# Kernel tuning notes

Hardware: AMD Instinct MI355X
Metric: run time of the kernel (lower is better)

Reference implementation:

```python
import jax, jax.numpy as jnp
import numpy as np
import math

H = 32      # num attention heads
KV = 8      # num key/value heads
D = 64      # head dim
ROPE_BASE = 10000.0


def _rope_cos_sin(seq_len, dtype):
    inv_freq = 1.0 / (ROPE_BASE ** (jnp.arange(0, D, 2, dtype=jnp.float32) / D))
    t = jnp.arange(seq_len, dtype=jnp.float32)
    freqs = jnp.einsum('i,j->ij', t, inv_freq)          # [S, D/2]
    emb = jnp.concatenate([freqs, freqs], axis=-1)       # [S, D]
    return jnp.cos(emb).astype(dtype)[None, None], jnp.sin(emb).astype(dtype)[None, None]


def _rotate_half(x):
    x1, x2 = x[..., : D // 2], x[..., D // 2:]
    return jnp.concatenate([-x2, x1], axis=-1)


def setup_inputs() -> dict:
    key = jax.random.key(0)
    ks = jax.random.split(key, 5)
    B, S, Hid = 1, 2048, 2048
    hidden_states = jax.random.normal(ks[0], (B, S, Hid), dtype=jnp.float32)
    Wq = jax.random.normal(ks[1], (Hid, H * D), dtype=jnp.float32) * (1.0 / math.sqrt(Hid))
    Wk = jax.random.normal(ks[2], (Hid, KV * D), dtype=jnp.float32) * (1.0 / math.sqrt(Hid))
    Wv = jax.random.normal(ks[3], (Hid, KV * D), dtype=jnp.float32) * (1.0 / math.sqrt(Hid))
    Wo = jax.random.normal(ks[4], (H * D, Hid), dtype=jnp.float32) * (1.0 / math.sqrt(H * D))
    # additive causal mask
    causal = jnp.tril(jnp.ones((S, S), dtype=bool))
    attention_mask = jnp.where(causal, 0.0, -1e9).astype(jnp.float32)[None, None]
    return {"hidden_states": hidden_states, "Wq": Wq, "Wk": Wk, "Wv": Wv,
            "Wo": Wo, "attention_mask": attention_mask}


def reference(hidden_states, Wq, Wk, Wv, Wo, attention_mask):
    B, S, _ = hidden_states.shape
    groups = H // KV
    # projections -> [B, heads, S, D]
    q = (hidden_states @ Wq).reshape(B, S, H, D).transpose(0, 2, 1, 3)
    k = (hidden_states @ Wk).reshape(B, S, KV, D).transpose(0, 2, 1, 3)
    v = (hidden_states @ Wv).reshape(B, S, KV, D).transpose(0, 2, 1, 3)
    # RoPE
    cos, sin = _rope_cos_sin(S, q.dtype)
    q = q * cos + _rotate_half(q) * sin
    k = k * cos + _rotate_half(k) * sin
    # GQA head expansion (repeat_interleave along head axis)
    k = jnp.repeat(k, groups, axis=1)
    v = jnp.repeat(v, groups, axis=1)
    # scaled dot-product attention (eager)
    scores = jnp.einsum('bhqd,bhkd->bhqk', q, k) / math.sqrt(D)
    scores = scores + attention_mask
    probs = jax.nn.softmax(scores.astype(jnp.float32), axis=-1).astype(q.dtype)
    attn = jnp.einsum('bhqk,bhkd->bhqd', probs, v)
    attn = attn.transpose(0, 2, 1, 3).reshape(B, S, H * D)
    return attn @ Wo
```

## Files before the change

kernel.cpp:

```cpp
#include <hip/hip_runtime.h>
#include <hip/hip_bf16.h>
#include <math.h>

#define S_LEN 2048
#define HID   2048
#define NH    32
#define NKV   8
#define HD    64
#define KVW   (NKV * HD)

typedef __attribute__((ext_vector_type(8))) short bf16x8;
typedef __attribute__((ext_vector_type(4))) float f32x4;
typedef unsigned short u16;

__device__ __forceinline__ u16 f2bf(float f) {
    return (u16)((__builtin_bit_cast(unsigned, f) + 0x8000u) >> 16);
}
__device__ __forceinline__ float bf2f(u16 v) {
    unsigned u = ((unsigned)v) << 16;
    return __builtin_bit_cast(float, u);
}
__device__ __forceinline__ unsigned pack2bf(float a, float b) {
    unsigned ua = __builtin_bit_cast(unsigned, a) + 0x8000u;
    unsigned ub = __builtin_bit_cast(unsigned, b) + 0x8000u;
    return (ua >> 16) | (ub & 0xFFFF0000u);
}
__device__ __forceinline__ void stage16(const u16* g, u16* lds_base) {
    __builtin_amdgcn_global_load_lds((const __attribute__((address_space(1))) void*)g,
                                     (__attribute__((address_space(3))) void*)lds_base, 16, 0, 0);
}

__global__ __launch_bounds__(256) void cvt_bf16x8_kernel(const float* __restrict__ X,
                                                         u16* __restrict__ Y, int n8) {
    int i = blockIdx.x * 256 + threadIdx.x;
    if (i >= n8) return;
    const float4* p = (const float4*)(X + (size_t)i * 8);
    float4 a = p[0], b = p[1];
    uint4 o;
    o.x = pack2bf(a.x, a.y);
    o.y = pack2bf(a.z, a.w);
    o.z = pack2bf(b.x, b.y);
    o.w = pack2bf(b.z, b.w);
    *(uint4*)(Y + (size_t)i * 8) = o;
}

__global__ __launch_bounds__(256) void transpose_cvt4(const float* __restrict__ Wq,
                                                      const float* __restrict__ Wk,
                                                      const float* __restrict__ Wv,
                                                      const float* __restrict__ Wo,
                                                      u16* __restrict__ WqkvT,
                                                      u16* __restrict__ WoT) {
    const float* X; u16* Y; int C;
    const int z = blockIdx.z;
    if (z == 0)      { X = Wq; Y = WqkvT;                        C = HID; }
    else if (z == 1) { X = Wo; Y = WoT;                          C = HID; }
    else if (z == 2) { X = Wk; Y = WqkvT + (size_t)2048 * HID;   C = KVW; }
    else             { X = Wv; Y = WqkvT + (size_t)2560 * HID;   C = KVW; }
    const int c0 = blockIdx.x * 32, r0 = blockIdx.y * 32;
    if (c0 >= C) return;
    __shared__ float T[32][33];
    const int tx = threadIdx.x & 31, ty = threadIdx.x >> 5;
#pragma unroll
    for (int i = 0; i < 4; i++)
        T[ty + 8 * i][tx] = X[(size_t)(r0 + ty + 8 * i) * C + c0 + tx];
    __syncthreads();
#pragma unroll
    for (int i = 0; i < 4; i++)
        Y[(size_t)(c0 + ty + 8 * i) * HID + r0 + tx] = f2bf(T[tx][ty + 8 * i]);
}

template <int EPI>
__global__ __launch_bounds__(512, 2) void gemm_bf16(const u16* __restrict__ A,
                                                    const u16* __restrict__ Bt,
                                                    float* __restrict__ C,
                                                    u16* __restrict__ Qh,
                                                    u16* __restrict__ Kh,
                                                    u16* __restrict__ Vt) {
    constexpr int KTOT = 2048;
    constexpr int NT = KTOT / 32;
    constexpr int SLOT = 12288;
    __shared__ u16 smem[4 * SLOT];

    const int tiles = gridDim.x * gridDim.y;
    const int flat = blockIdx.y * gridDim.x + blockIdx.x;
    const int per = tiles >> 3;
    const int swz = (flat & 7) * per + (flat >> 3);
    const int bxx = swz % gridDim.x, byy = swz / gridDim.x;
    const int bm = byy * 128, bn = bxx * 256;

    const int tid = threadIdx.x;
    const int w = tid >> 6, lane = tid & 63;
    const int qd = lane >> 4, r = lane & 15;
    const int wm = w >> 2, wn = w & 3;

    f32x4 acc[4][4];
#pragma unroll
    for (int m = 0; m < 4; m++)
#pragma unroll
        for (int n = 0; n < 4; n++) {
            acc[m][n][0] = 0.f; acc[m][n][1] = 0.f;
            acc[m][n][2] = 0.f; acc[m][n][3] = 0.f;
        }

    auto stage_tile = [&](int kt) {
        u16* slot = smem + (size_t)(kt & 3) * SLOT;
        const int k0 = kt * 32;
        const u16* ga = A + (size_t)(bm + w * 16 + r) * KTOT + k0 + qd * 8;
        stage16(ga, slot + w * 512);
        const u16* gb0 = Bt + (size_t)(bn + w * 16 + r) * KTOT + k0 + qd * 8;
        stage16(gb0, slot + 4096 + w * 512);
        const u16* gb1 = Bt + (size_t)(bn + (w + 8) * 16 + r) * KTOT + k0 + qd * 8;
        stage16(gb1, slot + 4096 + (w + 8) * 512);
    };

    auto compute_tile = [&](int kt) {
        const u16* slot = smem + (size_t)(kt & 3) * SLOT;
        bf16x8 af[4], bfv[4];
#pragma unroll
        for (int m = 0; m < 4; m++)
            af[m] = *(const bf16x8*)&slot[(wm * 4 + m) * 512 + lane * 8];
#pragma unroll
        for (int n = 0; n < 4; n++)
            bfv[n] = *(const bf16x8*)&slot[4096 + (wn * 4 + n) * 512 + lane * 8];
        __builtin_amdgcn_s_setprio(1);
#pragma unroll
        for (int m = 0; m < 4; m++)
#pragma unroll
            for (int n = 0; n < 4; n++)
                acc[m][n] = __builtin_amdgcn_mfma_f32_16x16x32_bf16(af[m], bfv[n], acc[m][n], 0, 0, 0);
        __builtin_amdgcn_s_setprio(0);
    };

#define VMB(n_) do { asm volatile("s_waitcnt vmcnt(" #n_ ")" ::: "memory");  \
                     __builtin_amdgcn_s_barrier();                           \
                     __builtin_amdgcn_sched_barrier(0); } while (0)

    stage_tile(0);
    stage_tile(1);
    stage_tile(2);

    for (int kt = 0; kt < NT - 3; ++kt) {
        VMB(6);
        stage_tile(kt + 3);
        __builtin_amdgcn_sched_barrier(0);
        compute_tile(kt);
    }
    VMB(6); compute_tile(NT - 3);
    VMB(3); compute_tile(NT - 2);
    VMB(0); compute_tile(NT - 1);
#undef VMB

    const int row0 = bm + wm * 64;
    const int col0 = bn + wn * 64;
    if (EPI == 0) {
#pragma unroll
        for (int m = 0; m < 4; m++)
#pragma unroll
            for (int n = 0; n < 4; n++)
#pragma unroll
                for (int reg = 0; reg < 4; reg++)
                    C[(size_t)(row0 + m * 16 + qd * 4 + reg) * HID + col0 + n * 16 + r] =
                        acc[m][n][reg];
    } else if (bn < 2048) {
#pragma unroll
        for (int m = 0; m < 4; m++)
#pragma unroll
            for (int n = 0; n < 4; n++)
#pragma unroll
                for (int reg = 0; reg < 4; reg++)
                    Qh[(size_t)(row0 + m * 16 + qd * 4 + reg) * HID + col0 + n * 16 + r] =
                        f2bf(acc[m][n][reg]);
    } else if (bn < 2560) {
        const int hb = (bn - 2048) + wn * 64;
#pragma unroll
        for (int n = 0; n < 2; n++) {
            const int c0 = n * 16 + r;
            const float inv = __expf(-(float)c0 * 0.2878231366242596f);
#pragma unroll
            for (int m = 0; m < 4; m++)
#pragma unroll
                for (int reg = 0; reg < 4; reg++) {
                    int srow = row0 + m * 16 + qd * 4 + reg;
                    float ang = (float)srow * inv;
                    float cs = cosf(ang), sn = sinf(ang);
                    float k1 = acc[m][n][reg], k2 = acc[m][n + 2][reg];
                    size_t o = (size_t)srow * KVW + hb + c0;
                    Kh[o]      = f2bf(k1 * cs - k2 * sn);
                    Kh[o + 32] = f2bf(k2 * cs + k1 * sn);
                }
        }
    } else {
#pragma unroll
        for (int m = 0; m < 4; m++)
#pragma unroll
            for (int n = 0; n < 4; n++) {
                int nrel = (bn - 2560) + wn * 64 + n * 16 + r;
                int m0 = row0 + m * 16 + qd * 4;
                ushort4 v;
                v.x = f2bf(acc[m][n][0]); v.y = f2bf(acc[m][n][1]);
                v.z = f2bf(acc[m][n][2]); v.w = f2bf(acc[m][n][3]);
                *(ushort4*)(Vt + (size_t)nrel * S_LEN + m0) = v;
            }
    }
}

__global__ __launch_bounds__(512, 6) void attn_mfma(const u16* __restrict__ Qh,
                                                    const u16* __restrict__ K,
                                                    const u16* __restrict__ Vt,
                                                    u16* __restrict__ O) {
    __shared__ u16 Kbuf[2][4096];
    __shared__ u16 Vbuf[4096];
    __shared__ u16 P_lds[8][16][72];

    const int w    = threadIdx.x >> 6;
    const int lane = threadIdx.x & 63;
    const int qd   = lane >> 4;
    const int r    = lane & 15;
    const int qb   = 15 - (int)blockIdx.x;
    const int h    = blockIdx.y;
    const int kvh  = h >> 2;
    const int q0w  = qb * 128 + w * 16;

    const u16* qrow = Qh + (size_t)(q0w + r) * (NH * HD) + h * HD;
    bf16x8 qlo = *(const bf16x8*)(qrow + qd * 8);
    bf16x8 qhi = *(const bf16x8*)(qrow + 32 + qd * 8);
    float y1[8], y2[8];
    const float spos = (float)(q0w + r);
    const float LN1E4_OVER_32 = 0.2878231366242596f;
#pragma unroll
    for (int i = 0; i < 8; i++) {
        int jj = qd * 8 + i;
        float x1 = bf2f((u16)qlo[i]);
        float x2 = bf2f((u16)qhi[i]);
        float inv = __expf(-(float)jj * LN1E4_OVER_32);
        float ang = spos * inv;
        float c = cosf(ang), sn = sinf(ang);
        y1[i] = (x1 * c - x2 * sn) * 0.125f;
        y2[i] = (x2 * c + x1 * sn) * 0.125f;
    }
    bf16x8 qfrag[2];
    {
        union { unsigned u[4]; bf16x8 v; } a, b;
#pragma unroll
        for (int i = 0; i < 4; i++) {
            a.u[i] = pack2bf(y1[2 * i], y1[2 * i + 1]);
            b.u[i] = pack2bf(y2[2 * i], y2[2 * i + 1]);
        }
        qfrag[0] = a.v; qfrag[1] = b.v;
    }

    bf16x8 ones;
    {
        union { u16 s[8]; bf16x8 v; } u;
#pragma unroll
        for (int i = 0; i < 8; i++) u.s[i] = 0x3F80;
        ones = u.v;
    }

    f32x4 oacc[4];
    f32x4 lacc;
#pragma unroll
    for (int i = 0; i < 4; i++) { oacc[i][0]=0.f; oacc[i][1]=0.f; oacc[i][2]=0.f; oacc[i][3]=0.f; }
    lacc[0]=0.f; lacc[1]=0.f; lacc[2]=0.f; lacc[3]=0.f;

    const int ktmax = 2 * qb + 1;

#define STAGE_K(kt_, buf_)                                                        \
    {                                                                             \
        const u16* g = K + (size_t)((kt_) * 64 + (w >> 1) * 16 + r) * KVW         \
                         + kvh * HD + (w & 1) * 32 + qd * 8;                      \
        stage16(g, &Kbuf[buf_][w * 512]);                                         \
    }
#define STAGE_V(kt_)                                                              \
    {                                                                             \
        const u16* g = Vt + (size_t)(kvh * HD + (w >> 1) * 16 + r) * S_LEN        \
                          + (kt_) * 64 + (w & 1) * 32 + qd * 8;                   \
        stage16(g, &Vbuf[w * 512]);                                               \
    }

    STAGE_K(0, 0);
    __syncthreads();
    int cur = 0;

    for (int kt = 0; kt <= ktmax; kt++) {
        STAGE_V(kt);
        if (kt < ktmax) STAGE_K(kt + 1, cur ^ 1);

        f32x4 s[4];
#pragma unroll
        for (int nt = 0; nt < 4; nt++) {
            bf16x8 kf0 = *(const bf16x8*)&Kbuf[cur][(nt * 2 + 0) * 512 + lane * 8];
            bf16x8 kf1 = *(const bf16x8*)&Kbuf[cur][(nt * 2 + 1) * 512 + lane * 8];
            f32x4 z; z[0]=0.f; z[1]=0.f; z[2]=0.f; z[3]=0.f;
            z = __builtin_amdgcn_mfma_f32_16x16x32_bf16(qfrag[0], kf0, z, 0, 0, 0);
            s[nt] = __builtin_amdgcn_mfma_f32_16x16x32_bf16(qfrag[1], kf1, z, 0, 0, 0);
        }

        if (kt * 64 + 63 > q0w) {
#pragma unroll
            for (int nt = 0; nt < 4; nt++) {
                int key = kt * 64 + nt * 16 + r;
#pragma unroll
                for (int reg = 0; reg < 4; reg++) {
                    int qg = q0w + qd * 4 + reg;
                    if (key > qg) s[nt][reg] = -1e30f;
                }
            }
        }

#pragma unroll
        for (int nt = 0; nt < 4; nt++)
#pragma unroll
            for (int reg = 0; reg < 4; reg++)
                P_lds[w][qd * 4 + reg][nt * 16 + r] = f2bf(__expf(s[nt][reg]));

        __syncthreads();

#pragma unroll
        for (int c = 0; c < 2; c++) {
            bf16x8 pf = *(const bf16x8*)&P_lds[w][r][c * 32 + qd * 8];
            lacc = __builtin_amdgcn_mfma_f32_16x16x32_bf16(pf, ones, lacc, 0, 0, 0);
#pragma unroll
            for (int ntd = 0; ntd < 4; ntd++) {
                bf16x8 vf = *(const bf16x8*)&Vbuf[(ntd * 2 + c) * 512 + lane * 8];
                oacc[ntd] = __builtin_amdgcn_mfma_f32_16x16x32_bf16(pf, vf, oacc[ntd], 0, 0, 0);
            }
        }

        __syncthreads();
        cur ^= 1;
    }
#undef STAGE_K
#undef STAGE_V

    float rl[4];
#pragma unroll
    for (int reg = 0; reg < 4; reg++) rl[reg] = 1.f / lacc[reg];
#pragma unroll
    for (int ntd = 0; ntd < 4; ntd++)
#pragma unroll
        for (int reg = 0; reg < 4; reg++)
            O[(size_t)(q0w + qd * 4 + reg) * (NH * HD) + h * HD + ntd * 16 + r] =
                f2bf(oacc[ntd][reg] * rl[reg]);
}

extern "C" void kernel_launch(void* const* d_in, const int* in_sizes, int n_in,
                              void* d_out, int out_size, void* d_ws, size_t ws_size,
                              hipStream_t stream) {
    const float* hidden = (const float*)d_in[0];
    const float* Wq = (const float*)d_in[1];
    const float* Wk = (const float*)d_in[2];
    const float* Wv = (const float*)d_in[3];
    const float* Wo = (const float*)d_in[4];
    float* out = (float*)d_out;

    char* ws = (char*)d_ws;
    const size_t MB = 1024 * 1024;
    u16* Hh     = (u16*)(ws + 0 * MB);
    u16* WqkvT  = (u16*)(ws + 8 * MB);
    u16* WoT    = (u16*)(ws + 20 * MB);
    u16* Qh     = (u16*)(ws + 28 * MB);
    u16* Kh     = (u16*)(ws + 36 * MB);
    u16* Vt     = (u16*)(ws + 38 * MB);
    u16* Ob     = WqkvT;

    cvt_bf16x8_kernel<<<(S_LEN * HID / 8 + 255) / 256, 256, 0, stream>>>(hidden, Hh, S_LEN * HID / 8);
    transpose_cvt4<<<dim3(HID / 32, HID / 32, 4), 256, 0, stream>>>(Wq, Wk, Wv, Wo, WqkvT, WoT);

    gemm_bf16<1><<<dim3(3072 / 256, S_LEN / 128), 512, 0, stream>>>(Hh, WqkvT, nullptr, Qh, Kh, Vt);

    attn_mfma<<<dim3(S_LEN / 128, NH), 512, 0, stream>>>(Qh, Kh, Vt, Ob);

    gemm_bf16<0><<<dim3(HID / 256, S_LEN / 128), 512, 0, stream>>>(Ob, WoT, out, nullptr, nullptr, nullptr);
}
```

Measured before the change: 288.8 us.

## Enlarge GEMM block tile to 256x256 with 64-wide K double buffering

Both GEMMs now use 256x256 output tiles per block, with 8x4 MFMA accumulators per warp, instead of 128x256. The 4-stage, 32-wide K ring buffer is replaced by a double-buffered 64-wide K stage using full vmcnt(0) waits and barriers. The aim is more operand reuse per LDS load and fewer loop iterations. In exchange the grid shrinks to 96 and 64 blocks, fewer than the CU count. LDS use also rises to 128KB, which limits occupancy and latency hiding.

```diff
diff --git a/kernel.cpp b/kernel.cpp
--- a/kernel.cpp
+++ b/kernel.cpp
@@ -75,86 +75,99 @@
                                                     float* __restrict__ C,
                                                     u16* __restrict__ Qh,
                                                     u16* __restrict__ Kh,
-                                                    u16* __restrict__ Vt) {
-    constexpr int KTOT = 2048;
-    constexpr int NT = KTOT / 32;
-    constexpr int SLOT = 12288;
-    __shared__ u16 smem[4 * SLOT];
+                                                    u16* __restrict__ Vt,
+                                                    int K) {
+    __shared__ u16 As[2][16384];
+    __shared__ u16 Bs[2][16384];
 
     const int tiles = gridDim.x * gridDim.y;
     const int flat = blockIdx.y * gridDim.x + blockIdx.x;
     const int per = tiles >> 3;
     const int swz = (flat & 7) * per + (flat >> 3);
     const int bxx = swz % gridDim.x, byy = swz / gridDim.x;
-    const int bm = byy * 128, bn = bxx * 256;
-
-    const int tid = threadIdx.x;
-    const int w = tid >> 6, lane = tid & 63;
+    const int bm = byy * 256, bn = bxx * 256;
+
+    const int t = threadIdx.x;
+    const int w = t >> 6, lane = t & 63;
     const int qd = lane >> 4, r = lane & 15;
     const int wm = w >> 2, wn = w & 3;
-
-    f32x4 acc[4][4];
-#pragma unroll
-    for (int m = 0; m < 4; m++)
+    const bool kblk = (EPI == 1) && (bn >= 2048) && (bn < 2560);
+    const int NT = K >> 6;
+
+    f32x4 acc[8][4];
+#pragma unroll
+    for (int m = 0; m < 8; m++)
 #pragma unroll
         for (int n = 0; n < 4; n++) {
             acc[m][n][0] = 0.f; acc[m][n][1] = 0.f;
             acc[m][n][2] = 0.f; acc[m][n][3] = 0.f;
         }
 
-    auto stage_tile = [&](int kt) {
-        u16* slot = smem + (size_t)(kt & 3) * SLOT;
-        const int k0 = kt * 32;
-        const u16* ga = A + (size_t)(bm + w * 16 + r) * KTOT + k0 + qd * 8;
-        stage16(ga, slot + w * 512);
-        const u16* gb0 = Bt + (size_t)(bn + w * 16 + r) * KTOT + k0 + qd * 8;
-        stage16(gb0, slot + 4096 + w * 512);
-        const u16* gb1 = Bt + (size_t)(bn + (w + 8) * 16 + r) * KTOT + k0 + qd * 8;
-        stage16(gb1, slot + 4096 + (w + 8) * 512);
-    };
-
-    auto compute_tile = [&](int kt) {
-        const u16* slot = smem + (size_t)(kt & 3) * SLOT;
-        bf16x8 af[4], bfv[4];
-#pragma unroll
-        for (int m = 0; m < 4; m++)
-            af[m] = *(const bf16x8*)&slot[(wm * 4 + m) * 512 + lane * 8];
-#pragma unroll
-        for (int n = 0; n < 4; n++)
-            bfv[n] = *(const bf16x8*)&slot[4096 + (wn * 4 + n) * 512 + lane * 8];
-        __builtin_amdgcn_s_setprio(1);
-#pragma unroll
-        for (int m = 0; m < 4; m++)
-#pragma unroll
-            for (int n = 0; n < 4; n++)
-                acc[m][n] = __builtin_amdgcn_mfma_f32_16x16x32_bf16(af[m], bfv[n], acc[m][n], 0, 0, 0);
-        __builtin_amdgcn_s_setprio(0);
-    };
-
-#define VMB(n_) do { asm volatile("s_waitcnt vmcnt(" #n_ ")" ::: "memory");  \
-                     __builtin_amdgcn_s_barrier();                           \
-                     __builtin_amdgcn_sched_barrier(0); } while (0)
-
-    stage_tile(0);
-    stage_tile(1);
-    stage_tile(2);
-
-    for (int kt = 0; kt < NT - 3; ++kt) {
-        VMB(6);
-        stage_tile(kt + 3);
-        __builtin_amdgcn_sched_barrier(0);
-        compute_tile(kt);
-    }
-    VMB(6); compute_tile(NT - 3);
-    VMB(3); compute_tile(NT - 2);
-    VMB(0); compute_tile(NT - 1);
-#undef VMB
-
-    const int row0 = bm + wm * 64;
+#define STAGE_TILE(kt_, s_)                                                       \
+    {                                                                             \
+        const int k0_ = (kt_) * 64;                                               \
+        _Pragma("unroll")                                                         \
+        for (int l = 0; l < 4; l++) {                                             \
+            const int chunk = w * 4 + l;                                          \
+            const int tt = chunk >> 1, ss = chunk & 1;                            \
+            const u16* ga = A + (size_t)(bm + tt * 16 + r) * K + k0_ + ss * 32 + qd * 8; \
+            stage16(ga, &As[s_][chunk * 512]);                                    \
+            const u16* gb = Bt + (size_t)(bn + tt * 16 + r) * K + k0_ + ss * 32 + qd * 8; \
+            stage16(gb, &Bs[s_][chunk * 512]);                                    \
+        }                                                                         \
+    }
+
+#define QUAD(s_, qm_, qn_)                                                        \
+    {                                                                             \
+        bf16x8 af[4][2], bfv[2][2];                                               \
+        _Pragma("unroll")                                                         \
+        for (int i = 0; i < 4; i++)                                               \
+            _Pragma("unroll")                                                     \
+            for (int kk = 0; kk < 2; kk++)                                        \
+                af[i][kk] = *(const bf16x8*)&As[s_][((wm * 8 + (qm_) * 4 + i) * 2 + kk) * 512 + lane * 8]; \
+        _Pragma("unroll")                                                         \
+        for (int j = 0; j < 2; j++)                                               \
+            _Pragma("unroll")                                                     \
+            for (int kk = 0; kk < 2; kk++)                                        \
+                bfv[j][kk] = *(const bf16x8*)&Bs[s_][((wn * 4 + (qn_) * 2 + j) * 2 + kk) * 512 + lane * 8]; \
+        __builtin_amdgcn_s_setprio(1);                                            \
+        _Pragma("unroll")                                                         \
+        for (int i = 0; i < 4; i++)                                               \
+            _Pragma("unroll")                                                     \
+            for (int j = 0; j < 2; j++)                                           \
+                _Pragma("unroll")                                                 \
+                for (int kk = 0; kk < 2; kk++)                                    \
+                    acc[(qm_) * 4 + i][(qn_) * 2 + j] =                           \
+                        __builtin_amdgcn_mfma_f32_16x16x32_bf16(af[i][kk], bfv[j][kk], \
+                            acc[(qm_) * 4 + i][(qn_) * 2 + j], 0, 0, 0);          \
+        __builtin_amdgcn_s_setprio(0);                                            \
+    }
+
+#define WAITBAR                                                                   \
+    asm volatile("s_waitcnt vmcnt(0)" ::: "memory");                              \
+    __builtin_amdgcn_s_barrier();
+
+    STAGE_TILE(0, 0);
+    WAITBAR;
+
+    for (int i2 = 0; i2 < NT / 2; ++i2) {
+        const int te = 2 * i2;
+        STAGE_TILE(te + 1, 1);
+        QUAD(0, 0, 0) QUAD(0, 0, 1) QUAD(0, 1, 0) QUAD(0, 1, 1)
+        WAITBAR;
+        if (te + 2 < NT) STAGE_TILE(te + 2, 0);
+        QUAD(1, 0, 0) QUAD(1, 0, 1) QUAD(1, 1, 0) QUAD(1, 1, 1)
+        WAITBAR;
+    }
+#undef STAGE_TILE
+#undef QUAD
+#undef WAITBAR
+
+    const int row0 = bm + wm * 128;
     const int col0 = bn + wn * 64;
     if (EPI == 0) {
 #pragma unroll
-        for (int m = 0; m < 4; m++)
+        for (int m = 0; m < 8; m++)
 #pragma unroll
             for (int n = 0; n < 4; n++)
 #pragma unroll
@@ -163,21 +176,21 @@
                         acc[m][n][reg];
     } else if (bn < 2048) {
 #pragma unroll
-        for (int m = 0; m < 4; m++)
+        for (int m = 0; m < 8; m++)
 #pragma unroll
             for (int n = 0; n < 4; n++)
 #pragma unroll
                 for (int reg = 0; reg < 4; reg++)
                     Qh[(size_t)(row0 + m * 16 + qd * 4 + reg) * HID + col0 + n * 16 + r] =
                         f2bf(acc[m][n][reg]);
-    } else if (bn < 2560) {
+    } else if (kblk) {
         const int hb = (bn - 2048) + wn * 64;
 #pragma unroll
         for (int n = 0; n < 2; n++) {
             const int c0 = n * 16 + r;
             const float inv = __expf(-(float)c0 * 0.2878231366242596f);
 #pragma unroll
-            for (int m = 0; m < 4; m++)
+            for (int m = 0; m < 8; m++)
 #pragma unroll
                 for (int reg = 0; reg < 4; reg++) {
                     int srow = row0 + m * 16 + qd * 4 + reg;
@@ -191,7 +204,7 @@
         }
     } else {
 #pragma unroll
-        for (int m = 0; m < 4; m++)
+        for (int m = 0; m < 8; m++)
 #pragma unroll
             for (int n = 0; n < 4; n++) {
                 int nrel = (bn - 2560) + wn * 64 + n * 16 + r;
@@ -367,9 +380,9 @@
     cvt_bf16x8_kernel<<<(S_LEN * HID / 8 + 255) / 256, 256, 0, stream>>>(hidden, Hh, S_LEN * HID / 8);
     transpose_cvt4<<<dim3(HID / 32, HID / 32, 4), 256, 0, stream>>>(Wq, Wk, Wv, Wo, WqkvT, WoT);
 
-    gemm_bf16<1><<<dim3(3072 / 256, S_LEN / 128), 512, 0, stream>>>(Hh, WqkvT, nullptr, Qh, Kh, Vt);
+    gemm_bf16<1><<<dim3(3072 / 256, S_LEN / 256), 512, 0, stream>>>(Hh, WqkvT, nullptr, Qh, Kh, Vt, HID);
 
     attn_mfma<<<dim3(S_LEN / 128, NH), 512, 0, stream>>>(Qh, Kh, Vt, Ob);
 
-    gemm_bf16<0><<<dim3(HID / 256, S_LEN / 128), 512, 0, stream>>>(Ob, WoT, out, nullptr, nullptr, nullptr);
-}
+    gemm_bf16<0><<<dim3(HID / 256, S_LEN / 256), 512, 0, stream>>>(Ob, WoT, out, nullptr, nullptr, nullptr, HID);
+}
```

Result: slower. 817.7 us (+183.1%).
